# Performance work log

Measured on AMD Instinct MI355X. Metric: run time of the kernel, lower is better.

## Reference

```python
import jax, jax.numpy as jnp
import numpy as np

EMBED_DIM = 12  # hardcoded in the original module


def setup_inputs() -> dict:
    key = jax.random.key(0)
    k_x, k_w, k_b, k_v = jax.random.split(key, 4)
    feature_dim = 768
    hidden_dim = 4
    feature_num = feature_dim // EMBED_DIM  # 64 fields
    batch = 32768
    x = jax.random.normal(k_x, (batch, feature_dim), dtype=jnp.float32)
    # nn.Linear(feature_dim, 1): weight [1, feature_dim], bias [1]
    W = jax.random.normal(k_w, (1, feature_dim), dtype=jnp.float32) / np.sqrt(feature_dim)
    b = jax.random.normal(k_b, (1,), dtype=jnp.float32) * 0.01
    # V: [feature_num, field_num, hidden_dim]
    V = jax.random.normal(k_v, (feature_num, feature_num, hidden_dim), dtype=jnp.float32)
    return {"x": x, "W": W, "b": b, "V": V}


def reference(x, W, b, V):
    B, D = x.shape
    F = V.shape[0]               # feature_num == field_num
    E = D // F                   # embedding_dim (12)
    # linear part: [B, 1]
    linear_part = x @ W.T + b
    # Pairwise interaction coefficients: C[i, j] = <V[i, j], V[j, i]>
    C = jnp.sum(V * jnp.swapaxes(V, 0, 1), axis=-1)          # [F, F]
    M = C * jnp.triu(jnp.ones((F, F), dtype=x.dtype), k=1)   # keep i < j only
    # sum_{i<j} (x_i . x_j) * C[i,j]  ==  sum_{j,e} Xr[b,j,e] * (sum_i Xr[b,i,e] * M[i,j])
    Xr = x.reshape(B, F, E)                                    # [B, F, E]
    T = jnp.einsum('bie,ij->bje', Xr, M)                       # [B, F, E]
    interaction = jnp.sum(Xr * T, axis=(1, 2))[:, None]        # [B, 1]
    return jax.nn.sigmoid(linear_part + interaction)
```

## Files before the change

kernel.cpp:

```cpp
#include <hip/hip_runtime.h>
#include <hip/hip_bf16.h>

#define BATCH 32768
#define NF    64
#define NE    12
#define MB    16
#define MROWS (MB*NE)
#define LSTR  68
#define NBLK  (BATCH/MB)

typedef __attribute__((ext_vector_type(8))) short short8;
typedef __attribute__((ext_vector_type(4))) float float4v;

#define WS_SHT 0
#define WS_SLT 8192
#define WS_WT  16384

__device__ __forceinline__ short bfb(float v) {
    union { __hip_bfloat16 h; short s; } u;
    u.h = __float2bfloat16(v);
    return u.s;
}

__global__ void prep_kernel(const float* __restrict__ V, const float* __restrict__ W,
                            unsigned short* __restrict__ ShT,
                            unsigned short* __restrict__ SlT,
                            float* __restrict__ WT) {
    const int idx = blockIdx.x * 256 + threadIdx.x;
    if (idx < NF * NF) {
        const int i = idx >> 6, j = idx & 63;
        const float4v a = *(const float4v*)(V + (size_t)((i << 6) | j) * 4);
        const float4v b = *(const float4v*)(V + (size_t)((j << 6) | i) * 4);
        const float s = (i == j) ? 0.0f
                      : 0.5f * (a.x * b.x + a.y * b.y + a.z * b.z + a.w * b.w);
        const __hip_bfloat16 sh = __float2bfloat16(s);
        union { __hip_bfloat16 h; unsigned short u; } uh, ul;
        uh.h = sh; ul.h = __float2bfloat16(s - __bfloat162float(sh));
        ShT[(j << 6) | i] = uh.u;
        SlT[(j << 6) | i] = ul.u;
    }
    if (idx < NF * NE) {
        const int j = idx / NE, e = idx - j * NE;
        WT[e * 64 + j] = W[idx];
    }
}

__global__ __launch_bounds__(256, 3) void ffm_mfma(
    const float* __restrict__ x,
    const float* __restrict__ bvec,
    const unsigned short* __restrict__ ShT,
    const unsigned short* __restrict__ SlT,
    const float* __restrict__ WT,
    float* __restrict__ out)
{
    __shared__ float Xs[MROWS * LSTR];
    __shared__ float red[MROWS];

    const int tid  = threadIdx.x;
    const int w    = tid >> 6;
    const int lane = tid & 63;
    const int l15  = lane & 15;
    const int q    = lane >> 4;

    const float4v* xg = (const float4v*)(x + (size_t)blockIdx.x * MB * (NF * NE));
    float4v v[12];
    #pragma unroll
    for (int p = 0; p < 12; ++p) v[p] = xg[p * 256 + tid];

    short8 shf[4][2], slf[4][2];
    #pragma unroll
    for (int ns = 0; ns < 4; ++ns)
        #pragma unroll
        for (int kb = 0; kb < 2; ++kb) {
            const int off = ((ns << 4) + l15) * 64 + kb * 32 + q * 8;
            shf[ns][kb] = *(const short8*)(ShT + off);
            slf[ns][kb] = *(const short8*)(SlT + off);
        }

    #pragma unroll
    for (int p = 0; p < 12; ++p) {
        const int fid = p * 256 + tid;
        const int b   = fid / 192;
        const int c4  = fid - b * 192;
        const int d0  = c4 * 4;
        const int i0  = d0 / 12;
        const int e0  = d0 - i0 * 12;
        float* dst = Xs + (b * NE + e0) * LSTR + i0;
        dst[0 * LSTR] = v[p].x; dst[1 * LSTR] = v[p].y;
        dst[2 * LSTR] = v[p].z; dst[3 * LSTR] = v[p].w;
    }
    __syncthreads();

    #pragma unroll
    for (int ms = 0; ms < 3; ++ms) {
        const int msg  = w * 3 + ms;
        const int mrow = (msg << 4) + l15;

        float av[16];
        #pragma unroll
        for (int kb = 0; kb < 2; ++kb) {
            const float4v t0 = *(const float4v*)(Xs + mrow * LSTR + kb * 32 + q * 8);
            const float4v t1 = *(const float4v*)(Xs + mrow * LSTR + kb * 32 + q * 8 + 4);
            av[kb*8+0]=t0.x; av[kb*8+1]=t0.y; av[kb*8+2]=t0.z; av[kb*8+3]=t0.w;
            av[kb*8+4]=t1.x; av[kb*8+5]=t1.y; av[kb*8+6]=t1.z; av[kb*8+7]=t1.w;
        }
        short8 ah[2], al[2];
        #pragma unroll
        for (int kb = 0; kb < 2; ++kb)
            #pragma unroll
            for (int j = 0; j < 8; ++j) {
                const float vv = av[kb * 8 + j];
                const __hip_bfloat16 h = __float2bfloat16(vv);
                ah[kb][j] = bfb(vv);
                al[kb][j] = bfb(vv - __bfloat162float(h));
            }

        float4v acc[4];
        #pragma unroll
        for (int ns = 0; ns < 4; ++ns) {
            float4v c = (float4v){0.f, 0.f, 0.f, 0.f};
            c = __builtin_amdgcn_mfma_f32_16x16x32_bf16(ah[0], shf[ns][0], c, 0, 0, 0);
            c = __builtin_amdgcn_mfma_f32_16x16x32_bf16(ah[1], shf[ns][1], c, 0, 0, 0);
            c = __builtin_amdgcn_mfma_f32_16x16x32_bf16(al[0], shf[ns][0], c, 0, 0, 0);
            c = __builtin_amdgcn_mfma_f32_16x16x32_bf16(al[1], shf[ns][1], c, 0, 0, 0);
            c = __builtin_amdgcn_mfma_f32_16x16x32_bf16(ah[0], slf[ns][0], c, 0, 0, 0);
            c = __builtin_amdgcn_mfma_f32_16x16x32_bf16(ah[1], slf[ns][1], c, 0, 0, 0);
            acc[ns] = c;
        }

        #pragma unroll
        for (int rg = 0; rg < 4; ++rg) {
            const int m = (msg << 4) + (q << 2) + rg;
            const int e = m % NE;
            float p = 0.0f;
            #pragma unroll
            for (int ns = 0; ns < 4; ++ns) {
                const int n = (ns << 4) + l15;
                p = fmaf(Xs[m * LSTR + n], acc[ns][rg] + WT[e * 64 + n], p);
            }
            p += __shfl_xor(p, 1);
            p += __shfl_xor(p, 2);
            p += __shfl_xor(p, 4);
            p += __shfl_xor(p, 8);
            if (l15 == 0) red[m] = p;
        }
    }
    __syncthreads();

    if (tid < MB) {
        float s = 0.0f;
        #pragma unroll
        for (int e = 0; e < NE; ++e) s += red[tid * NE + e];
        const float z = s + bvec[0];
        out[blockIdx.x * MB + tid] = 1.0f / (1.0f + __expf(-z));
    }
}

extern "C" void kernel_launch(void* const* d_in, const int* in_sizes, int n_in,
                              void* d_out, int out_size, void* d_ws, size_t ws_size,
                              hipStream_t stream) {
    const float* x  = (const float*)d_in[0];
    const float* W  = (const float*)d_in[1];
    const float* bb = (const float*)d_in[2];
    const float* V  = (const float*)d_in[3];
    unsigned short* ShT = (unsigned short*)((char*)d_ws + WS_SHT);
    unsigned short* SlT = (unsigned short*)((char*)d_ws + WS_SLT);
    float*          WT  = (float*)((char*)d_ws + WS_WT);
    float* out = (float*)d_out;

    prep_kernel<<<dim3(16), dim3(256), 0, stream>>>(V, W, ShT, SlT, WT);
    ffm_mfma<<<dim3(NBLK), dim3(256), 0, stream>>>(x, bb, ShT, SlT, WT, out);
}
```

Measured before the change: 165.9 us.

## Fold linear weights into MFMA B matrix and rebuild X via identity MFMA

Extends the bf16 hi/lo coefficient matrix with 16 extra columns, 12 holding the linear weights W and 4 zero padding, so the linear term comes out of the same MFMA pass. The epilogue no longer reads Xs values and WT from shared and global memory. It rebuilds the transposed X tile in registers by multiplying the split bf16 A fragments with an identity matrix through MFMA. This removes scattered LDS and global loads in the epilogue but adds 8 identity MFMAs and one extra 6-MFMA tile per subtile. The reconstructed X now carries only hi+lo bf16 precision instead of exact fp32.

After: 156.6 us. 5.6% less time.

```diff
diff --git a/kernel.cpp b/kernel.cpp
--- a/kernel.cpp
+++ b/kernel.cpp
@@ -4,6 +4,7 @@
 #define BATCH 32768
 #define NF    64
 #define NE    12
+#define NEXT  80
 #define MB    16
 #define MROWS (MB*NE)
 #define LSTR  68
@@ -12,9 +13,8 @@
 typedef __attribute__((ext_vector_type(8))) short short8;
 typedef __attribute__((ext_vector_type(4))) float float4v;
 
-#define WS_SHT 0
-#define WS_SLT 8192
-#define WS_WT  16384
+#define WS_BHT 0
+#define WS_BLT 10240
 
 __device__ __forceinline__ short bfb(float v) {
     union { __hip_bfloat16 h; short s; } u;
@@ -23,34 +23,33 @@
 }
 
 __global__ void prep_kernel(const float* __restrict__ V, const float* __restrict__ W,
-                            unsigned short* __restrict__ ShT,
-                            unsigned short* __restrict__ SlT,
-                            float* __restrict__ WT) {
+                            unsigned short* __restrict__ BhT,
+                            unsigned short* __restrict__ BlT) {
     const int idx = blockIdx.x * 256 + threadIdx.x;
-    if (idx < NF * NF) {
-        const int i = idx >> 6, j = idx & 63;
-        const float4v a = *(const float4v*)(V + (size_t)((i << 6) | j) * 4);
-        const float4v b = *(const float4v*)(V + (size_t)((j << 6) | i) * 4);
-        const float s = (i == j) ? 0.0f
-                      : 0.5f * (a.x * b.x + a.y * b.y + a.z * b.z + a.w * b.w);
-        const __hip_bfloat16 sh = __float2bfloat16(s);
-        union { __hip_bfloat16 h; unsigned short u; } uh, ul;
-        uh.h = sh; ul.h = __float2bfloat16(s - __bfloat162float(sh));
-        ShT[(j << 6) | i] = uh.u;
-        SlT[(j << 6) | i] = ul.u;
+    if (idx >= NEXT * NF) return;
+    const int n = idx >> 6, k = idx & 63;
+    float v = 0.0f;
+    if (n < 64) {
+        if (k != n) {
+            const float4v a = *(const float4v*)(V + (size_t)((k << 6) | n) * 4);
+            const float4v b = *(const float4v*)(V + (size_t)((n << 6) | k) * 4);
+            v = 0.5f * (a.x * b.x + a.y * b.y + a.z * b.z + a.w * b.w);
+        }
+    } else if (n < 76) {
+        v = W[k * NE + (n - 64)];
     }
-    if (idx < NF * NE) {
-        const int j = idx / NE, e = idx - j * NE;
-        WT[e * 64 + j] = W[idx];
-    }
+    const __hip_bfloat16 h = __float2bfloat16(v);
+    union { __hip_bfloat16 h; unsigned short u; } uh, ul;
+    uh.h = h; ul.h = __float2bfloat16(v - __bfloat162float(h));
+    BhT[idx] = uh.u;
+    BlT[idx] = ul.u;
 }
 
 __global__ __launch_bounds__(256, 3) void ffm_mfma(
     const float* __restrict__ x,
     const float* __restrict__ bvec,
-    const unsigned short* __restrict__ ShT,
-    const unsigned short* __restrict__ SlT,
-    const float* __restrict__ WT,
+    const unsigned short* __restrict__ BhT,
+    const unsigned short* __restrict__ BlT,
     float* __restrict__ out)
 {
     __shared__ float Xs[MROWS * LSTR];
@@ -67,15 +66,22 @@
     #pragma unroll
     for (int p = 0; p < 12; ++p) v[p] = xg[p * 256 + tid];
 
-    short8 shf[4][2], slf[4][2];
+    short8 shf[5][2], slf[5][2];
     #pragma unroll
-    for (int ns = 0; ns < 4; ++ns)
+    for (int ns = 0; ns < 5; ++ns)
         #pragma unroll
         for (int kb = 0; kb < 2; ++kb) {
             const int off = ((ns << 4) + l15) * 64 + kb * 32 + q * 8;
-            shf[ns][kb] = *(const short8*)(ShT + off);
-            slf[ns][kb] = *(const short8*)(SlT + off);
+            shf[ns][kb] = *(const short8*)(BhT + off);
+            slf[ns][kb] = *(const short8*)(BlT + off);
         }
+
+    short8 If[2];
+    #pragma unroll
+    for (int h = 0; h < 2; ++h)
+        #pragma unroll
+        for (int j = 0; j < 8; ++j)
+            If[h][j] = (q * 8 + j == h * 16 + l15) ? (short)0x3F80 : (short)0;
 
     #pragma unroll
     for (int p = 0; p < 12; ++p) {
@@ -96,28 +102,34 @@
         const int msg  = w * 3 + ms;
         const int mrow = (msg << 4) + l15;
 
-        float av[16];
+        short8 ah[2], al[2];
         #pragma unroll
         for (int kb = 0; kb < 2; ++kb) {
             const float4v t0 = *(const float4v*)(Xs + mrow * LSTR + kb * 32 + q * 8);
             const float4v t1 = *(const float4v*)(Xs + mrow * LSTR + kb * 32 + q * 8 + 4);
-            av[kb*8+0]=t0.x; av[kb*8+1]=t0.y; av[kb*8+2]=t0.z; av[kb*8+3]=t0.w;
-            av[kb*8+4]=t1.x; av[kb*8+5]=t1.y; av[kb*8+6]=t1.z; av[kb*8+7]=t1.w;
-        }
-        short8 ah[2], al[2];
-        #pragma unroll
-        for (int kb = 0; kb < 2; ++kb)
+            const float a8[8] = {t0.x, t0.y, t0.z, t0.w, t1.x, t1.y, t1.z, t1.w};
             #pragma unroll
             for (int j = 0; j < 8; ++j) {
-                const float vv = av[kb * 8 + j];
+                const float vv = a8[j];
                 const __hip_bfloat16 h = __float2bfloat16(vv);
                 ah[kb][j] = bfb(vv);
                 al[kb][j] = bfb(vv - __bfloat162float(h));
             }
+        }
 
-        float4v acc[4];
+        float4v y1[4];
         #pragma unroll
         for (int ns = 0; ns < 4; ++ns) {
+            const int kb = ns >> 1;
+            float4v c = (float4v){0.f, 0.f, 0.f, 0.f};
+            c = __builtin_amdgcn_mfma_f32_16x16x32_bf16(ah[kb], If[ns & 1], c, 0, 0, 0);
+            c = __builtin_amdgcn_mfma_f32_16x16x32_bf16(al[kb], If[ns & 1], c, 0, 0, 0);
+            y1[ns] = c;
+        }
+
+        float pv[4] = {0.f, 0.f, 0.f, 0.f};
+        #pragma unroll
+        for (int ns = 0; ns < 5; ++ns) {
             float4v c = (float4v){0.f, 0.f, 0.f, 0.f};
             c = __builtin_amdgcn_mfma_f32_16x16x32_bf16(ah[0], shf[ns][0], c, 0, 0, 0);
             c = __builtin_amdgcn_mfma_f32_16x16x32_bf16(ah[1], shf[ns][1], c, 0, 0, 0);
@@ -125,24 +137,28 @@
             c = __builtin_amdgcn_mfma_f32_16x16x32_bf16(al[1], shf[ns][1], c, 0, 0, 0);
             c = __builtin_amdgcn_mfma_f32_16x16x32_bf16(ah[0], slf[ns][0], c, 0, 0, 0);
             c = __builtin_amdgcn_mfma_f32_16x16x32_bf16(ah[1], slf[ns][1], c, 0, 0, 0);
-            acc[ns] = c;
+            if (ns < 4) {
+                #pragma unroll
+                for (int rg = 0; rg < 4; ++rg)
+                    pv[rg] = fmaf(y1[ns][rg], c[rg], pv[rg]);
+            } else {
+                #pragma unroll
+                for (int rg = 0; rg < 4; ++rg) {
+                    const int m = (msg << 4) + (q << 2) + rg;
+                    const int e = m % NE;
+                    pv[rg] += (l15 == e) ? c[rg] : 0.0f;
+                }
+            }
         }
 
         #pragma unroll
         for (int rg = 0; rg < 4; ++rg) {
-            const int m = (msg << 4) + (q << 2) + rg;
-            const int e = m % NE;
-            float p = 0.0f;
-            #pragma unroll
-            for (int ns = 0; ns < 4; ++ns) {
-                const int n = (ns << 4) + l15;
-                p = fmaf(Xs[m * LSTR + n], acc[ns][rg] + WT[e * 64 + n], p);
-            }
+            float p = pv[rg];
             p += __shfl_xor(p, 1);
             p += __shfl_xor(p, 2);
             p += __shfl_xor(p, 4);
             p += __shfl_xor(p, 8);
-            if (l15 == 0) red[m] = p;
+            if (l15 == 0) red[(msg << 4) + (q << 2) + rg] = p;
         }
     }
     __syncthreads();
@@ -163,11 +179,10 @@
     const float* W  = (const float*)d_in[1];
     const float* bb = (const float*)d_in[2];
     const float* V  = (const float*)d_in[3];
-    unsigned short* ShT = (unsigned short*)((char*)d_ws + WS_SHT);
-    unsigned short* SlT = (unsigned short*)((char*)d_ws + WS_SLT);
-    float*          WT  = (float*)((char*)d_ws + WS_WT);
+    unsigned short* BhT = (unsigned short*)((char*)d_ws + WS_BHT);
+    unsigned short* BlT = (unsigned short*)((char*)d_ws + WS_BLT);
     float* out = (float*)d_out;
 
-    prep_kernel<<<dim3(16), dim3(256), 0, stream>>>(V, W, ShT, SlT, WT);
-    ffm_mfma<<<dim3(NBLK), dim3(256), 0, stream>>>(x, bb, ShT, SlT, WT, out);
+    prep_kernel<<<dim3(20), dim3(256), 0, stream>>>(V, W, BhT, BlT);
+    ffm_mfma<<<dim3(NBLK), dim3(256), 0, stream>>>(x, bb, BhT, BlT, out);
 }
```
